# Kernel tuning notes

Measured on AMD Instinct MI355X. Metric: run time of the kernel, lower is better.

The kernel has to match this reference:

```python
import jax, jax.numpy as jnp
import numpy as np

S, B, H = 4096, 64, 256
D = 2.0
SIGMA = D / 2.0


def setup_inputs() -> dict:
    key = jax.random.key(0)
    ks = jax.random.split(key, 7)
    return {
        "e": jax.random.normal(ks[0], (S, B, H), dtype=jnp.float32),
        "d": jax.random.normal(ks[1], (1, B, H), dtype=jnp.float32),
        "W_a": jax.random.normal(ks[2], (H, H), dtype=jnp.float32) / np.sqrt(H),
        "W_p": jax.random.normal(ks[3], (H, H), dtype=jnp.float32) / np.sqrt(H),
        "v_p": jax.random.normal(ks[4], (H, 1), dtype=jnp.float32) / np.sqrt(H),
        "lin_w": jax.random.normal(ks[5], (H, 2 * H), dtype=jnp.float32) / np.sqrt(2 * H),
        "lin_b": jax.random.normal(ks[6], (H,), dtype=jnp.float32) * 0.01,
    }


def reference(e, d, W_a, W_p, v_p, lin_w, lin_b):
    s = e.shape[0]
    # alignment: scores over source positions, softmax along S (dim 0 in torch)
    scores = jnp.sum((d @ W_a) * e, axis=2)          # [S, B]
    a = jax.nn.softmax(scores, axis=0)               # [S, B]
    # predictive position gating (Luong local-p attention)
    h = jnp.tanh(d[0] @ W_p)                         # [B, H]
    p_center = jax.nn.sigmoid((h @ v_p)[:, 0])[None, :] * s   # [1, B]
    pos = jnp.arange(s, dtype=e.dtype)[:, None]      # [S, 1]
    diff = p_center - pos                            # [S, B]
    mask = (jnp.abs(diff) <= D).astype(e.dtype)
    p = jnp.exp(-(diff * diff) / (2.0 * SIGMA * SIGMA)) * mask  # [S, B]
    w = a * p                                        # [S, B]
    context = jnp.einsum('sbh,sb->bh', e, w)[None]   # [1, B, H]
    x = jnp.concatenate([context, d], axis=2)        # [1, B, 2H]
    out = jax.nn.relu(x @ lin_w.T + lin_b)           # dropout = identity (eval)
    return out, w
```

## Files before the change

### kernel.cpp

```cpp
#include <hip/hip_runtime.h>
#include <math.h>

constexpr int S_ = 4096;
constexpr int B_ = 64;
constexpr int H_ = 256;
constexpr int NB_ = 1024;
constexpr float SHIFT = 60.0f;


__global__ __launch_bounds__(1024) void kA_prep(const float* __restrict__ d,
                                                const float* __restrict__ W_a,
                                                const float* __restrict__ W_p,
                                                const float* __restrict__ v_p,
                                                float* __restrict__ dW,
                                                float* __restrict__ pc) {
  const int b = blockIdx.x;
  const int t = threadIdx.x;
  const int h = t & 255;
  const int kc = t >> 8;
  const float* db = d + b * H_;
  float aa = 0.f, ap = 0.f;
#pragma unroll 8
  for (int k = kc * 64; k < kc * 64 + 64; ++k) {
    float dv = db[k];
    aa = fmaf(dv, W_a[k * H_ + h], aa);
    ap = fmaf(dv, W_p[k * H_ + h], ap);
  }
  __shared__ float redA[1024];
  __shared__ float redB[1024];
  redA[t] = aa;
  redB[t] = ap;
  __syncthreads();
  if (t < 256) {
    float dwa = redA[t] + redA[t + 256] + redA[t + 512] + redA[t + 768];
    float dwp = redB[t] + redB[t + 256] + redB[t + 512] + redB[t + 768];
    dW[b * H_ + t] = dwa;
    redA[t] = tanhf(dwp) * v_p[t];
  }
  __syncthreads();
  for (int st = 128; st > 0; st >>= 1) {
    if (t < st) redA[t] += redA[t + st];
    __syncthreads();
  }
  if (t == 0) pc[b] = (float)S_ / (1.f + expf(-redA[0]));
}

__global__ __launch_bounds__(256) void kB_scores(const float* __restrict__ e,
                                                 const float* __restrict__ dW,
                                                 const float* __restrict__ pc,
                                                 float* __restrict__ lpart,
                                                 float* __restrict__ swin,
                                                 float* __restrict__ w_out) {
  int t = threadIdx.x;
  int wave = t >> 6;
  int lane = t & 63;
  int bl = lane >> 2;
  int sub = lane & 3;
  int b = wave * 16 + bl;
  int s0 = blockIdx.x * 4;

  const float4* dW4 = (const float4*)(dW + b * H_);
  float4 wreg[16];
#pragma unroll
  for (int j = 0; j < 16; ++j) wreg[j] = dW4[sub + 4 * j];

  __shared__ float tile[4][64];
#pragma unroll
  for (int r = 0; r < 4; ++r) {
    const float4* erow = (const float4*)(e + ((size_t)(s0 + r) * B_ + b) * H_);
    float acc = 0.f;
#pragma unroll
    for (int half = 0; half < 2; ++half) {
      float4 ev[8];
#pragma unroll
      for (int j = 0; j < 8; ++j) ev[j] = erow[sub + 4 * (half * 8 + j)];
#pragma unroll
      for (int j = 0; j < 8; ++j) {
        const float4 wv = wreg[half * 8 + j];
        acc = fmaf(ev[j].x, wv.x, fmaf(ev[j].y, wv.y,
              fmaf(ev[j].z, wv.z, fmaf(ev[j].w, wv.w, acc))));
      }
    }
    acc += __shfl_xor(acc, 1, 64);
    acc += __shfl_xor(acc, 2, 64);
    if (sub == 0) tile[r][b] = acc;
  }
  __syncthreads();
  if (t < 64) {
    const int bb = t;
    float lp = expf(tile[0][bb] - SHIFT) + expf(tile[1][bb] - SHIFT) +
               expf(tile[2][bb] - SHIFT) + expf(tile[3][bb] - SHIFT);
    lpart[bb * NB_ + blockIdx.x] = lp;
    const float pcb = pc[bb];
#pragma unroll
    for (int r = 0; r < 4; ++r) {
      int s = s0 + r;
      if (fabsf(pcb - (float)s) <= 2.f) swin[bb * 8 + (s & 7)] = tile[r][bb];
    }
  }
  {
    int r = t >> 6, bz = t & 63;
    w_out[(size_t)(s0 + r) * B_ + bz] = 0.f;
  }
}

__global__ __launch_bounds__(1024) void kD_out(const float* __restrict__ lpart,
                                               const float* __restrict__ swin,
                                               const float* __restrict__ pcv,
                                               const float* __restrict__ e,
                                               const float* __restrict__ d,
                                               const float* __restrict__ lin_w,
                                               const float* __restrict__ lin_b,
                                               float* __restrict__ out,
                                               float* __restrict__ w_out) {
  const int b = blockIdx.x;
  const int t = threadIdx.x;
  __shared__ float red[1024];
  red[t] = lpart[b * NB_ + t];
  __syncthreads();
  for (int st = 512; st > 0; st >>= 1) {
    if (t < st) red[t] += red[t + st];
    __syncthreads();
  }
  const float invL = 1.f / red[0];
  const float pcb = pcv[b];
  const int s0 = max(0, (int)ceilf(pcb - 2.f));
  const int s1 = min(S_ - 1, (int)floorf(pcb + 2.f));
  const int nw = s1 - s0 + 1;
  __shared__ float wsh[8];
  __shared__ float xbuf[512];
  if (t < nw) {
    const int s = s0 + t;
    const float diff = pcb - (float)s;
    const float w = expf(swin[b * 8 + (s & 7)] - SHIFT) * invL * expf(-0.5f * diff * diff);
    w_out[(size_t)s * B_ + b] = w;
    wsh[t] = w;
  }
  __syncthreads();
  if (t < 256) {
    float ctx = 0.f;
    for (int j = 0; j < nw; ++j)
      ctx = fmaf(wsh[j], e[((size_t)(s0 + j) * B_ + b) * H_ + t], ctx);
    xbuf[t] = ctx;
    xbuf[256 + t] = d[b * H_ + t];
  }
  __syncthreads();
  const int h = t >> 2, part = t & 3;
  const float4* lw = (const float4*)(lin_w + h * 2 * H_) + part * 32;
  const float4* xv = (const float4*)xbuf + part * 32;
  float acc = 0.f;
#pragma unroll 8
  for (int k = 0; k < 32; ++k) {
    float4 a4 = lw[k];
    float4 b4 = xv[k];
    acc += a4.x * b4.x + a4.y * b4.y + a4.z * b4.z + a4.w * b4.w;
  }
  red[t] = acc;
  __syncthreads();
  if (t < 256) {
    float r = red[4 * t] + red[4 * t + 1] + red[4 * t + 2] + red[4 * t + 3] + lin_b[t];
    out[b * H_ + t] = fmaxf(r, 0.f);
  }
}

extern "C" void kernel_launch(void* const* d_in, const int* in_sizes, int n_in,
                              void* d_out, int out_size, void* d_ws, size_t ws_size,
                              hipStream_t stream) {
  const float* e     = (const float*)d_in[0];
  const float* dd    = (const float*)d_in[1];
  const float* W_a   = (const float*)d_in[2];
  const float* W_p   = (const float*)d_in[3];
  const float* v_p   = (const float*)d_in[4];
  const float* lin_w = (const float*)d_in[5];
  const float* lin_b = (const float*)d_in[6];

  float* out   = (float*)d_out;
  float* w_out = out + B_ * H_;

  float* ws    = (float*)d_ws;
  float* dW    = ws;
  float* pc    = ws + 16384;
  float* swin  = ws + 16448;
  float* lpart = ws + 16960;

  kA_prep<<<B_, 1024, 0, stream>>>(dd, W_a, W_p, v_p, dW, pc);
  kB_scores<<<NB_, 256, 0, stream>>>(e, dW, pc, lpart, swin, w_out);
  kD_out<<<B_, 1024, 0, stream>>>(lpart, swin, pc, e, dd, lin_w, lin_b, out, w_out);
}
```

Measured before the change: 71.16 us.

## Fuse output stage into score kernel with atomic counter and last-block finalization

Merges the final output kernel into the scores kernel. Partial softmax sums are accumulated with atomics, window scores are published with atomicExch, and the last 64 blocks to finish (tracked by a global counter) spin-wait until every block has arrived, then each computes one batch's context and linear output. Zeroing of the weight output moves into the prep kernel, and a memset resets the accumulators. This removes one launch and the lpart reduction, at the cost of atomic contention and a spin-wait whose safety depends on all blocks being resident or having already retired.

```diff
diff --git a/kernel.cpp b/kernel.cpp
--- a/kernel.cpp
+++ b/kernel.cpp
@@ -13,7 +13,8 @@
                                                 const float* __restrict__ W_p,
                                                 const float* __restrict__ v_p,
                                                 float* __restrict__ dW,
-                                                float* __restrict__ pc) {
+                                                float* __restrict__ pc,
+                                                float* __restrict__ w_out) {
   const int b = blockIdx.x;
   const int t = threadIdx.x;
   const int h = t & 255;
@@ -25,6 +26,10 @@
     float dv = db[k];
     aa = fmaf(dv, W_a[k * H_ + h], aa);
     ap = fmaf(dv, W_p[k * H_ + h], ap);
+  }
+  {
+    float4 z = make_float4(0.f, 0.f, 0.f, 0.f);
+    ((float4*)w_out)[blockIdx.x * 1024 + t] = z;
   }
   __shared__ float redA[1024];
   __shared__ float redB[1024];
@@ -45,85 +50,85 @@
   if (t == 0) pc[b] = (float)S_ / (1.f + expf(-redA[0]));
 }
 
-__global__ __launch_bounds__(256) void kB_scores(const float* __restrict__ e,
-                                                 const float* __restrict__ dW,
-                                                 const float* __restrict__ pc,
-                                                 float* __restrict__ lpart,
-                                                 float* __restrict__ swin,
-                                                 float* __restrict__ w_out) {
-  int t = threadIdx.x;
-  int wave = t >> 6;
-  int lane = t & 63;
-  int bl = lane >> 2;
-  int sub = lane & 3;
-  int b = wave * 16 + bl;
-  int s0 = blockIdx.x * 4;
+__global__ __launch_bounds__(256) void kB_fused(const float* __restrict__ e,
+                                                const float* __restrict__ dW,
+                                                const float* __restrict__ pc,
+                                                const float* __restrict__ d,
+                                                const float* __restrict__ lin_w,
+                                                const float* __restrict__ lin_b,
+                                                float* __restrict__ Lacc,
+                                                float* __restrict__ swinG,
+                                                unsigned int* __restrict__ counter,
+                                                float* __restrict__ out,
+                                                float* __restrict__ w_out) {
+  const int t = threadIdx.x;
+  const int blk = blockIdx.x;
+  __shared__ float tile[4][64];
+  __shared__ unsigned int ordS;
 
-  const float4* dW4 = (const float4*)(dW + b * H_);
-  float4 wreg[16];
+  {
+    const int wave = t >> 6, lane = t & 63;
+    const int bl = lane >> 2, sub = lane & 3;
+    const int b = wave * 16 + bl;
+    const int s0 = blk * 4;
+    const float4* dW4 = (const float4*)(dW + b * H_);
+    float4 wreg[16];
 #pragma unroll
-  for (int j = 0; j < 16; ++j) wreg[j] = dW4[sub + 4 * j];
-
-  __shared__ float tile[4][64];
+    for (int j = 0; j < 16; ++j) wreg[j] = dW4[sub + 4 * j];
 #pragma unroll
-  for (int r = 0; r < 4; ++r) {
-    const float4* erow = (const float4*)(e + ((size_t)(s0 + r) * B_ + b) * H_);
-    float acc = 0.f;
+    for (int r = 0; r < 4; ++r) {
+      const float4* erow = (const float4*)(e + ((size_t)(s0 + r) * B_ + b) * H_);
+      float acc = 0.f;
 #pragma unroll
-    for (int half = 0; half < 2; ++half) {
-      float4 ev[8];
+      for (int half = 0; half < 2; ++half) {
+        float4 ev[8];
 #pragma unroll
-      for (int j = 0; j < 8; ++j) ev[j] = erow[sub + 4 * (half * 8 + j)];
+        for (int j = 0; j < 8; ++j) ev[j] = erow[sub + 4 * (half * 8 + j)];
 #pragma unroll
-      for (int j = 0; j < 8; ++j) {
-        const float4 wv = wreg[half * 8 + j];
-        acc = fmaf(ev[j].x, wv.x, fmaf(ev[j].y, wv.y,
-              fmaf(ev[j].z, wv.z, fmaf(ev[j].w, wv.w, acc))));
+        for (int j = 0; j < 8; ++j) {
+          const float4 wv = wreg[half * 8 + j];
+          acc = fmaf(ev[j].x, wv.x, fmaf(ev[j].y, wv.y,
+                fmaf(ev[j].z, wv.z, fmaf(ev[j].w, wv.w, acc))));
+        }
       }
+      acc += __shfl_xor(acc, 1, 64);
+      acc += __shfl_xor(acc, 2, 64);
+      if (sub == 0) tile[r][b] = acc;
     }
-    acc += __shfl_xor(acc, 1, 64);
-    acc += __shfl_xor(acc, 2, 64);
-    if (sub == 0) tile[r][b] = acc;
   }
   __syncthreads();
   if (t < 64) {
     const int bb = t;
+    const int s0 = blk * 4;
     float lp = expf(tile[0][bb] - SHIFT) + expf(tile[1][bb] - SHIFT) +
                expf(tile[2][bb] - SHIFT) + expf(tile[3][bb] - SHIFT);
-    lpart[bb * NB_ + blockIdx.x] = lp;
+    atomicAdd(&Lacc[bb * 16], lp);
     const float pcb = pc[bb];
 #pragma unroll
     for (int r = 0; r < 4; ++r) {
       int s = s0 + r;
-      if (fabsf(pcb - (float)s) <= 2.f) swin[bb * 8 + (s & 7)] = tile[r][bb];
+      if (fabsf(pcb - (float)s) <= 2.f)
+        atomicExch(&swinG[bb * 8 + (s & 7)], tile[r][bb]);
     }
   }
-  {
-    int r = t >> 6, bz = t & 63;
-    w_out[(size_t)(s0 + r) * B_ + bz] = 0.f;
+  __syncthreads();
+  if (t == 0) ordS = atomicAdd(counter, 1u);
+  __syncthreads();
+  const unsigned int ord = ordS;
+  if (ord < (unsigned)(NB_ - B_)) return;
+  const int bf = (int)(ord - (NB_ - B_));
+
+  if (t == 0) {
+    while (__hip_atomic_load(counter, __ATOMIC_RELAXED, __HIP_MEMORY_SCOPE_AGENT)
+           < (unsigned)NB_)
+      __builtin_amdgcn_s_sleep(2);
   }
-}
+  __syncthreads();
 
-__global__ __launch_bounds__(1024) void kD_out(const float* __restrict__ lpart,
-                                               const float* __restrict__ swin,
-                                               const float* __restrict__ pcv,
-                                               const float* __restrict__ e,
-                                               const float* __restrict__ d,
-                                               const float* __restrict__ lin_w,
-                                               const float* __restrict__ lin_b,
-                                               float* __restrict__ out,
-                                               float* __restrict__ w_out) {
-  const int b = blockIdx.x;
-  const int t = threadIdx.x;
-  __shared__ float red[1024];
-  red[t] = lpart[b * NB_ + t];
-  __syncthreads();
-  for (int st = 512; st > 0; st >>= 1) {
-    if (t < st) red[t] += red[t + st];
-    __syncthreads();
-  }
-  const float invL = 1.f / red[0];
-  const float pcb = pcv[b];
+  const float pcb = pc[bf];
+  const float L = __hip_atomic_load(&Lacc[bf * 16], __ATOMIC_RELAXED,
+                                    __HIP_MEMORY_SCOPE_AGENT);
+  const float invL = 1.f / L;
   const int s0 = max(0, (int)ceilf(pcb - 2.f));
   const int s1 = min(S_ - 1, (int)floorf(pcb + 2.f));
   const int nw = s1 - s0 + 1;
@@ -132,34 +137,32 @@
   if (t < nw) {
     const int s = s0 + t;
     const float diff = pcb - (float)s;
-    const float w = expf(swin[b * 8 + (s & 7)] - SHIFT) * invL * expf(-0.5f * diff * diff);
-    w_out[(size_t)s * B_ + b] = w;
+    const float sw = __hip_atomic_load(&swinG[bf * 8 + (s & 7)], __ATOMIC_RELAXED,
+                                       __HIP_MEMORY_SCOPE_AGENT);
+    const float w = expf(sw - SHIFT) * invL * expf(-0.5f * diff * diff);
+    w_out[(size_t)s * B_ + bf] = w;
     wsh[t] = w;
   }
   __syncthreads();
-  if (t < 256) {
+  {
     float ctx = 0.f;
     for (int j = 0; j < nw; ++j)
-      ctx = fmaf(wsh[j], e[((size_t)(s0 + j) * B_ + b) * H_ + t], ctx);
+      ctx = fmaf(wsh[j], e[((size_t)(s0 + j) * B_ + bf) * H_ + t], ctx);
     xbuf[t] = ctx;
-    xbuf[256 + t] = d[b * H_ + t];
+    xbuf[256 + t] = d[bf * H_ + t];
   }
   __syncthreads();
-  const int h = t >> 2, part = t & 3;
-  const float4* lw = (const float4*)(lin_w + h * 2 * H_) + part * 32;
-  const float4* xv = (const float4*)xbuf + part * 32;
-  float acc = 0.f;
+  {
+    float acc = lin_b[t];
+    const float4* lw = (const float4*)(lin_w + t * 2 * H_);
+    const float4* xv = (const float4*)xbuf;
 #pragma unroll 8
-  for (int k = 0; k < 32; ++k) {
-    float4 a4 = lw[k];
-    float4 b4 = xv[k];
-    acc += a4.x * b4.x + a4.y * b4.y + a4.z * b4.z + a4.w * b4.w;
-  }
-  red[t] = acc;
-  __syncthreads();
-  if (t < 256) {
-    float r = red[4 * t] + red[4 * t + 1] + red[4 * t + 2] + red[4 * t + 3] + lin_b[t];
-    out[b * H_ + t] = fmaxf(r, 0.f);
+    for (int k = 0; k < 128; ++k) {
+      float4 a4 = lw[k];
+      float4 b4 = xv[k];
+      acc += a4.x * b4.x + a4.y * b4.y + a4.z * b4.z + a4.w * b4.w;
+    }
+    out[bf * H_ + t] = fmaxf(acc, 0.f);
   }
 }
 
@@ -180,10 +183,12 @@
   float* ws    = (float*)d_ws;
   float* dW    = ws;
   float* pc    = ws + 16384;
-  float* swin  = ws + 16448;
-  float* lpart = ws + 16960;
+  float* Lacc  = ws + 16448;
+  unsigned int* counter = (unsigned int*)(ws + 17472);
+  float* swinG = ws + 17536;
 
-  kA_prep<<<B_, 1024, 0, stream>>>(dd, W_a, W_p, v_p, dW, pc);
-  kB_scores<<<NB_, 256, 0, stream>>>(e, dW, pc, lpart, swin, w_out);
-  kD_out<<<B_, 1024, 0, stream>>>(lpart, swin, pc, e, dd, lin_w, lin_b, out, w_out);
+  hipMemsetAsync(ws + 16448, 0, (17536 - 16448) * sizeof(float), stream);
+  kA_prep<<<B_, 1024, 0, stream>>>(dd, W_a, W_p, v_p, dW, pc, w_out);
+  kB_fused<<<NB_, 256, 0, stream>>>(e, dW, pc, dd, lin_w, lin_b,
+                                    Lacc, swinG, counter, out, w_out);
 }
```

Measured after the change: 87.47 us. 1.23x slower.

## Fuse prep into score kernel, per-batch chunking, recompute window scores in output kernel

Applied to the files above, without the earlier changes.

Removes the separate prep kernel by having each score block recompute d@W_a for its batch, and moves the W_p/position computation into the final kernel. Score blocks now handle one batch over a 256-row chunk, writing 16 partial sums per batch instead of 1024. The final kernel recomputes the few window scores directly rather than reading stored ones. This saves one launch and a dependency stage but repeats the d@W_a matvec in every block (16x per batch), and each block's e accesses are now strided rows of a single batch.

```diff
diff --git a/kernel.cpp b/kernel.cpp
--- a/kernel.cpp
+++ b/kernel.cpp
@@ -4,70 +4,67 @@
 constexpr int S_ = 4096;
 constexpr int B_ = 64;
 constexpr int H_ = 256;
-constexpr int NB_ = 1024;
+constexpr int NCH = 16;
+constexpr int ROWS = S_ / NCH;
 constexpr float SHIFT = 60.0f;
 
 
-__global__ __launch_bounds__(1024) void kA_prep(const float* __restrict__ d,
-                                                const float* __restrict__ W_a,
-                                                const float* __restrict__ W_p,
-                                                const float* __restrict__ v_p,
-                                                float* __restrict__ dW,
-                                                float* __restrict__ pc) {
-  const int b = blockIdx.x;
+__global__ __launch_bounds__(256) void kMain(const float* __restrict__ e,
+                                             const float* __restrict__ d,
+                                             const float* __restrict__ W_a,
+                                             float* __restrict__ dW,
+                                             float* __restrict__ lpart,
+                                             float* __restrict__ w_out) {
+  const int bid = blockIdx.x;
+  const int b = bid & 63;
+  const int c = bid >> 6;
   const int t = threadIdx.x;
-  const int h = t & 255;
-  const int kc = t >> 8;
-  const float* db = d + b * H_;
-  float aa = 0.f, ap = 0.f;
+  const int w = t >> 6;
+  const int lane = t & 63;
+
+  __shared__ float4 part[4][64];
+  __shared__ float4 dw4[64];
+  __shared__ float lred[64];
+
+  {
+    const float* db = d + b * H_;
+    const float4* Wa4 = (const float4*)W_a;
+    float4 acc = make_float4(0.f, 0.f, 0.f, 0.f);
 #pragma unroll 8
-  for (int k = kc * 64; k < kc * 64 + 64; ++k) {
-    float dv = db[k];
-    aa = fmaf(dv, W_a[k * H_ + h], aa);
-    ap = fmaf(dv, W_p[k * H_ + h], ap);
-  }
-  __shared__ float redA[1024];
-  __shared__ float redB[1024];
-  redA[t] = aa;
-  redB[t] = ap;
-  __syncthreads();
-  if (t < 256) {
-    float dwa = redA[t] + redA[t + 256] + redA[t + 512] + redA[t + 768];
-    float dwp = redB[t] + redB[t + 256] + redB[t + 512] + redB[t + 768];
-    dW[b * H_ + t] = dwa;
-    redA[t] = tanhf(dwp) * v_p[t];
-  }
-  __syncthreads();
-  for (int st = 128; st > 0; st >>= 1) {
-    if (t < st) redA[t] += redA[t + st];
-    __syncthreads();
-  }
-  if (t == 0) pc[b] = (float)S_ / (1.f + expf(-redA[0]));
-}
-
-__global__ __launch_bounds__(256) void kB_scores(const float* __restrict__ e,
-                                                 const float* __restrict__ dW,
-                                                 const float* __restrict__ pc,
-                                                 float* __restrict__ lpart,
-                                                 float* __restrict__ swin,
-                                                 float* __restrict__ w_out) {
-  int t = threadIdx.x;
-  int wave = t >> 6;
-  int lane = t & 63;
-  int bl = lane >> 2;
-  int sub = lane & 3;
-  int b = wave * 16 + bl;
-  int s0 = blockIdx.x * 4;
-
-  const float4* dW4 = (const float4*)(dW + b * H_);
+    for (int i = 0; i < 64; ++i) {
+      const int k = w * 64 + i;
+      const float dv = db[k];
+      const float4 wa = Wa4[k * 64 + lane];
+      acc.x = fmaf(dv, wa.x, acc.x);
+      acc.y = fmaf(dv, wa.y, acc.y);
+      acc.z = fmaf(dv, wa.z, acc.z);
+      acc.w = fmaf(dv, wa.w, acc.w);
+    }
+    part[w][lane] = acc;
+    __syncthreads();
+    if (t < 64) {
+      float4 a0 = part[0][t], a1 = part[1][t], a2 = part[2][t], a3 = part[3][t];
+      float4 r = make_float4(a0.x + a1.x + a2.x + a3.x,
+                             a0.y + a1.y + a2.y + a3.y,
+                             a0.z + a1.z + a2.z + a3.z,
+                             a0.w + a1.w + a2.w + a3.w);
+      dw4[t] = r;
+      if (c == 0) ((float4*)(dW + b * H_))[t] = r;
+    }
+    __syncthreads();
+  }
+
+  const int rr = lane >> 2;
+  const int sub = lane & 3;
   float4 wreg[16];
 #pragma unroll
-  for (int j = 0; j < 16; ++j) wreg[j] = dW4[sub + 4 * j];
-
-  __shared__ float tile[4][64];
-#pragma unroll
-  for (int r = 0; r < 4; ++r) {
-    const float4* erow = (const float4*)(e + ((size_t)(s0 + r) * B_ + b) * H_);
+  for (int j = 0; j < 16; ++j) wreg[j] = dw4[sub + 4 * j];
+
+  float lsum = 0.f;
+#pragma unroll 1
+  for (int p = 0; p < 4; ++p) {
+    const int s = c * ROWS + p * 64 + w * 16 + rr;
+    const float4* erow = (const float4*)(e + ((size_t)s * B_ + b) * H_);
     float acc = 0.f;
 #pragma unroll
     for (int half = 0; half < 2; ++half) {
@@ -83,58 +80,86 @@
     }
     acc += __shfl_xor(acc, 1, 64);
     acc += __shfl_xor(acc, 2, 64);
-    if (sub == 0) tile[r][b] = acc;
-  }
+    if (sub == 0) lsum += expf(acc - SHIFT);
+  }
+  if (sub == 0) lred[w * 16 + rr] = lsum;
   __syncthreads();
   if (t < 64) {
-    const int bb = t;
-    float lp = expf(tile[0][bb] - SHIFT) + expf(tile[1][bb] - SHIFT) +
-               expf(tile[2][bb] - SHIFT) + expf(tile[3][bb] - SHIFT);
-    lpart[bb * NB_ + blockIdx.x] = lp;
-    const float pcb = pc[bb];
-#pragma unroll
-    for (int r = 0; r < 4; ++r) {
-      int s = s0 + r;
-      if (fabsf(pcb - (float)s) <= 2.f) swin[bb * 8 + (s & 7)] = tile[r][bb];
-    }
-  }
-  {
-    int r = t >> 6, bz = t & 63;
-    w_out[(size_t)(s0 + r) * B_ + bz] = 0.f;
-  }
+    float v = lred[t];
+#pragma unroll
+    for (int off = 32; off > 0; off >>= 1) v += __shfl_xor(v, off, 64);
+    if (t == 0) lpart[b * NCH + c] = v;
+  }
+  w_out[bid * 256 + t] = 0.f;
 }
 
-__global__ __launch_bounds__(1024) void kD_out(const float* __restrict__ lpart,
-                                               const float* __restrict__ swin,
-                                               const float* __restrict__ pcv,
-                                               const float* __restrict__ e,
-                                               const float* __restrict__ d,
-                                               const float* __restrict__ lin_w,
-                                               const float* __restrict__ lin_b,
-                                               float* __restrict__ out,
-                                               float* __restrict__ w_out) {
+__global__ __launch_bounds__(1024) void kD(const float* __restrict__ e,
+                                           const float* __restrict__ d,
+                                           const float* __restrict__ W_p,
+                                           const float* __restrict__ v_p,
+                                           const float* __restrict__ lin_w,
+                                           const float* __restrict__ lin_b,
+                                           const float* __restrict__ dW,
+                                           const float* __restrict__ lpart,
+                                           float* __restrict__ out,
+                                           float* __restrict__ w_out) {
   const int b = blockIdx.x;
   const int t = threadIdx.x;
   __shared__ float red[1024];
-  red[t] = lpart[b * NB_ + t];
-  __syncthreads();
-  for (int st = 512; st > 0; st >>= 1) {
-    if (t < st) red[t] += red[t + st];
-    __syncthreads();
-  }
-  const float invL = 1.f / red[0];
-  const float pcb = pcv[b];
+  __shared__ float sstate[2];
+  __shared__ float scW[8];
+  __shared__ float wsh[8];
+  __shared__ float xbuf[512];
+
+  {
+    const int h = t & 255, kc = t >> 8;
+    const float* db = d + b * H_;
+    float ap = 0.f;
+#pragma unroll 8
+    for (int k = kc * 64; k < kc * 64 + 64; ++k)
+      ap = fmaf(db[k], W_p[k * H_ + h], ap);
+    red[t] = ap;
+    __syncthreads();
+    if (t < 256) {
+      float sp = red[t] + red[t + 256] + red[t + 512] + red[t + 768];
+      red[t] = tanhf(sp) * v_p[t];
+    }
+    __syncthreads();
+    for (int st = 128; st > 0; st >>= 1) {
+      if (t < st) red[t] += red[t + st];
+      __syncthreads();
+    }
+    if (t == 0) {
+      sstate[0] = (float)S_ / (1.f + expf(-red[0]));
+      float L = 0.f;
+#pragma unroll
+      for (int j = 0; j < NCH; ++j) L += lpart[b * NCH + j];
+      sstate[1] = 1.f / L;
+    }
+    __syncthreads();
+  }
+  const float pcb = sstate[0];
+  const float invL = sstate[1];
   const int s0 = max(0, (int)ceilf(pcb - 2.f));
   const int s1 = min(S_ - 1, (int)floorf(pcb + 2.f));
   const int nw = s1 - s0 + 1;
-  __shared__ float wsh[8];
-  __shared__ float xbuf[512];
+
+  if (t < nw * 64) {
+    const int j = t >> 6, lane = t & 63;
+    const float4 ev = ((const float4*)(e + ((size_t)(s0 + j) * B_ + b) * H_))[lane];
+    const float4 wv = ((const float4*)(dW + b * H_))[lane];
+    float p = ev.x * wv.x + ev.y * wv.y + ev.z * wv.z + ev.w * wv.w;
+#pragma unroll
+    for (int off = 32; off > 0; off >>= 1) p += __shfl_xor(p, off, 64);
+    if (lane == 0) scW[j] = p;
+  }
+  __syncthreads();
   if (t < nw) {
     const int s = s0 + t;
     const float diff = pcb - (float)s;
-    const float w = expf(swin[b * 8 + (s & 7)] - SHIFT) * invL * expf(-0.5f * diff * diff);
-    w_out[(size_t)s * B_ + b] = w;
-    wsh[t] = w;
+    const float wv = expf(scW[t] - SHIFT) * invL * expf(-0.5f * diff * diff);
+    wsh[t] = wv;
+    w_out[(size_t)s * B_ + b] = wv;
   }
   __syncthreads();
   if (t < 256) {
@@ -145,14 +170,13 @@
     xbuf[256 + t] = d[b * H_ + t];
   }
   __syncthreads();
-  const int h = t >> 2, part = t & 3;
-  const float4* lw = (const float4*)(lin_w + h * 2 * H_) + part * 32;
-  const float4* xv = (const float4*)xbuf + part * 32;
+  const int h = t >> 2, prt = t & 3;
+  const float4* lw = (const float4*)(lin_w + h * 2 * H_) + prt * 32;
+  const float4* xv = (const float4*)xbuf + prt * 32;
   float acc = 0.f;
 #pragma unroll 8
   for (int k = 0; k < 32; ++k) {
-    float4 a4 = lw[k];
-    float4 b4 = xv[k];
+    float4 a4 = lw[k], b4 = xv[k];
     acc += a4.x * b4.x + a4.y * b4.y + a4.z * b4.z + a4.w * b4.w;
   }
   red[t] = acc;
@@ -179,11 +203,8 @@
 
   float* ws    = (float*)d_ws;
   float* dW    = ws;
-  float* pc    = ws + 16384;
-  float* swin  = ws + 16448;
-  float* lpart = ws + 16960;
-
-  kA_prep<<<B_, 1024, 0, stream>>>(dd, W_a, W_p, v_p, dW, pc);
-  kB_scores<<<NB_, 256, 0, stream>>>(e, dW, pc, lpart, swin, w_out);
-  kD_out<<<B_, 1024, 0, stream>>>(lpart, swin, pc, e, dd, lin_w, lin_b, out, w_out);
+  float* lpart = ws + 16384;
+
+  kMain<<<B_ * NCH, 256, 0, stream>>>(e, dd, W_a, dW, lpart, w_out);
+  kD<<<B_, 1024, 0, stream>>>(e, dd, W_p, v_p, lin_w, lin_b, dW, lpart, out, w_out);
 }
```

Measured after the change: 69.67 us, median of 2. 1.02x faster.
